# Kernel optimization log

Measured on AMD Instinct MI355X. Metric: run time of the kernel, lower is better.

## Reference

```python
import jax, jax.numpy as jnp
import numpy as np

B, N, K, D = 4, 2048, 32, 256
TOKEN_DIM = 256
EGO_DIM = 256
NUM_HEADS = 4
LN_EPS = 1e-6


def masked_softmax(logits, mask, axis):
    mask = mask.astype(jnp.bool_)
    while mask.ndim < logits.ndim:
        mask = mask[..., None]
    neg_big = jnp.finfo(logits.dtype).min
    has_any = jnp.any(mask, axis=axis, keepdims=True)
    masked_logits = jnp.where(mask, logits, neg_big)
    masked_logits = jnp.where(has_any, masked_logits, 0.0)
    weights = jax.nn.softmax(masked_logits, axis=axis)
    weights = jnp.where(mask, weights, 0.0)
    denom = jnp.sum(weights, axis=axis, keepdims=True)
    weights = jnp.where(denom > 0, weights / denom, 0.0)
    return weights


def setup_inputs() -> dict:
    key = jax.random.key(0)
    ks = jax.random.split(key, 10)
    inv_tok = jax.random.normal(ks[0], (B, N, K, D), dtype=jnp.float32)
    ego_ctx = jax.random.normal(ks[1], (B, N, EGO_DIM), dtype=jnp.float32)
    r = jax.random.normal(ks[2], (B, N, K, 3), dtype=jnp.float32)
    u = jax.random.normal(ks[3], (B, N, K, 3), dtype=jnp.float32)
    mask = jax.random.randint(ks[4], (B, N, K), 0, 2).astype(jnp.bool_)
    # params
    W_ego = jax.random.normal(ks[5], (EGO_DIM, TOKEN_DIM), dtype=jnp.float32) * 0.05
    b_ego = jnp.zeros((TOKEN_DIM,), dtype=jnp.float32)
    ln_scale = jnp.ones((D,), dtype=jnp.float32)
    ln_bias = jnp.zeros((D,), dtype=jnp.float32)
    W_h = jax.random.normal(ks[6], (D + TOKEN_DIM, TOKEN_DIM), dtype=jnp.float32) * 0.05
    b_h = jnp.zeros((TOKEN_DIM,), dtype=jnp.float32)
    W_logit = jax.random.normal(ks[7], (TOKEN_DIM, NUM_HEADS), dtype=jnp.float32) * 0.01
    b_logit = jnp.zeros((NUM_HEADS,), dtype=jnp.float32)
    return {"inv_tok": inv_tok, "ego_ctx": ego_ctx, "r": r, "u": u, "mask": mask,
            "W_ego": W_ego, "b_ego": b_ego, "ln_scale": ln_scale, "ln_bias": ln_bias,
            "W_h": W_h, "b_h": b_h, "W_logit": W_logit, "b_logit": b_logit}


def reference(inv_tok, ego_ctx, r, u, mask, W_ego, b_ego, ln_scale, ln_bias, W_h, b_h, W_logit, b_logit):
    # ego context projection, broadcast over K
    ego_h = ego_ctx @ W_ego + b_ego                      # (B,N,T)
    ego_b = jnp.broadcast_to(ego_h[:, :, None, :], (B, N, K, TOKEN_DIM))
    # LayerNorm over last axis of inv_tok
    mean = jnp.mean(inv_tok, axis=-1, keepdims=True)
    var = jnp.var(inv_tok, axis=-1, keepdims=True)
    ln = (inv_tok - mean) * jax.lax.rsqrt(var + LN_EPS) * ln_scale + ln_bias
    h = jnp.concatenate([ln, ego_b], axis=-1)            # (B,N,K,D+T)
    h = jax.nn.gelu(h @ W_h + b_h, approximate=True)     # (B,N,K,T)
    logits = h @ W_logit + b_logit                       # (B,N,K,H)
    alpha = masked_softmax(logits, mask, axis=-2)        # (B,N,K,H)
    v_r = jnp.einsum('bnkh,bnkd->bnhd', alpha, r).reshape(B, N, 3 * NUM_HEADS)
    v_u = jnp.einsum('bnkh,bnkd->bnhd', alpha, u).reshape(B, N, 3 * NUM_HEADS)
    return (v_r, v_u, alpha)
```

## Files before the change

kernel.cpp:

```cpp
#include <hip/hip_runtime.h>

typedef float f32x4 __attribute__((ext_vector_type(4)));
typedef short bf16x8 __attribute__((ext_vector_type(8)));

__device__ __forceinline__ unsigned short f2bf(float f){
    unsigned int u = __builtin_bit_cast(unsigned int, f);
    u = u + 0x7fffu + ((u >> 16) & 1u);
    return (unsigned short)(u >> 16);
}
__device__ __forceinline__ float bf2f(unsigned short h){
    unsigned int u = ((unsigned int)h) << 16;
    return __builtin_bit_cast(float, u);
}
__device__ __forceinline__ unsigned int pk2_rtz(float a, float b){
    unsigned int ua = __builtin_bit_cast(unsigned int, a);
    unsigned int ub = __builtin_bit_cast(unsigned int, b);
    return (ua >> 16) | (ub & 0xffff0000u);
}
__device__ __forceinline__ unsigned short bfrtz(float a){
    return (unsigned short)(__builtin_bit_cast(unsigned int, a) >> 16);
}
__device__ __forceinline__ float gelu_f(float x){
    float t = x * x;
    float u = fmaf(0.044715f, t, 1.0f);
    float y = 1.5957691216057308f * x * u;
    float e = __expf(-y);
    return x * __builtin_amdgcn_rcpf(1.0f + e);
}

__device__ __forceinline__ int packpos(int k, int n, int NT){
    int kt = k >> 5, quad = (k >> 3) & 3, j = k & 7;
    int nt = n >> 4, nl = n & 15;
    return ((kt * NT + nt) * 64 + quad * 16 + nl) * 8 + j;
}

__global__ __launch_bounds__(256) void prep(const float* __restrict__ Wh,
        const float* __restrict__ Wlogit, const float* __restrict__ Wego,
        const float* __restrict__ b_ego, const float* __restrict__ b_h,
        const float* __restrict__ ln_s, const float* __restrict__ ln_b,
        unsigned short* __restrict__ Bp1, unsigned short* __restrict__ BpL,
        unsigned short* __restrict__ Bpc, float* __restrict__ b_combo,
        float* __restrict__ v1){
    __shared__ float rowbuf[512];
    int bid = blockIdx.x, tid = threadIdx.x;
    if (bid < 64){
        int base = (bid * 256 + tid) * 4;
        int k = base >> 8;
        float sc = ln_s[k];
        for (int e = base; e < base + 4; ++e){
            int n = e & 255;
            Bp1[packpos(k, n, 16)] = f2bf(sc * Wh[k * 256 + n]);
        }
    } else if (bid == 64){
        for (int e = tid * 16; e < tid * 16 + 16; ++e){
            int k = e >> 4, n = e & 15;
            float v = (n < 4) ? Wlogit[k * 4 + n] : 0.0f;
            BpL[packpos(k, n, 1)] = f2bf(v);
        }
    } else if (bid == 65){
        rowbuf[tid]       = b_ego[tid];
        rowbuf[256 + tid] = ln_b[tid];
        __syncthreads();
        float acc = b_h[tid];
        for (int j = 0; j < 256; ++j) acc += rowbuf[j] * Wh[(256 + j) * 256 + tid];
        for (int k = 0; k < 256; ++k) acc += rowbuf[256 + k] * Wh[k * 256 + tid];
        b_combo[tid] = acc;
    } else if (bid == 66){
        rowbuf[tid] = ln_s[tid];
        __syncthreads();
        float acc = 0.f;
        for (int k = 0; k < 256; ++k)
            acc += bf2f(f2bf(rowbuf[k] * Wh[k * 256 + tid]));
        v1[tid] = acc;
    } else {
        int k = bid - 67;
        rowbuf[tid] = Wego[k * 256 + tid];
        __syncthreads();
        float acc = 0.f;
        const float4* row4 = (const float4*)rowbuf;
        for (int j4 = 0; j4 < 64; ++j4){
            float4 e = row4[j4];
            int j = j4 * 4;
            acc += e.x * Wh[(256 + j) * 256 + tid];
            acc += e.y * Wh[(257 + j) * 256 + tid];
            acc += e.z * Wh[(258 + j) * 256 + tid];
            acc += e.w * Wh[(259 + j) * 256 + tid];
        }
        Bpc[packpos(k, tid, 16)] = f2bf(acc);
    }
}

__global__ __launch_bounds__(256) void ego_gemm(const float* __restrict__ ego_ctx,
        const unsigned short* __restrict__ Bpc, const float* __restrict__ b_combo,
        unsigned short* __restrict__ ego_term){
    const int tid = threadIdx.x, w = tid >> 6, l = tid & 63;
    const int m0 = blockIdx.x * 16;
    const int row = m0 + (l & 15);
    const int kq = (l >> 4) << 3;
    f32x4 acc[4];
    #pragma unroll
    for (int j = 0; j < 4; ++j) acc[j] = 0;
    #pragma unroll
    for (int kt = 0; kt < 8; ++kt){
        const float* ap = ego_ctx + row * 256 + kt * 32 + kq;
        float4 x0 = *(const float4*)ap;
        float4 x1 = *(const float4*)(ap + 4);
        unsigned int ua[4];
        ua[0] = ((unsigned int)f2bf(x0.x)) | ((unsigned int)f2bf(x0.y) << 16);
        ua[1] = ((unsigned int)f2bf(x0.z)) | ((unsigned int)f2bf(x0.w) << 16);
        ua[2] = ((unsigned int)f2bf(x1.x)) | ((unsigned int)f2bf(x1.y) << 16);
        ua[3] = ((unsigned int)f2bf(x1.z)) | ((unsigned int)f2bf(x1.w) << 16);
        bf16x8 a = __builtin_bit_cast(bf16x8, *(uint4*)ua);
        #pragma unroll
        for (int j = 0; j < 4; ++j){
            int nt = w * 4 + j;
            bf16x8 b = *(const bf16x8*)&Bpc[((kt * 16 + nt) * 64 + l) * 8];
            acc[j] = __builtin_amdgcn_mfma_f32_16x16x32_bf16(a, b, acc[j], 0, 0, 0);
        }
    }
    const int rq = (l >> 4) << 2, colc = l & 15;
    #pragma unroll
    for (int j = 0; j < 4; ++j){
        int n = (w * 4 + j) * 16 + colc;
        float bc = b_combo[n];
        #pragma unroll
        for (int rg = 0; rg < 4; ++rg)
            ego_term[(m0 + rq + rg) * 256 + n] = f2bf(acc[j][rg] + bc);
    }
}

__global__ __launch_bounds__(256) void main_fused(const float* __restrict__ inv,
        const float* __restrict__ rin, const float* __restrict__ uin,
        const int* __restrict__ mask, const float* __restrict__ b_logit,
        const unsigned short* __restrict__ Bp1, const unsigned short* __restrict__ BpL,
        const unsigned short* __restrict__ ego_term, const float* __restrict__ v1g,
        float* __restrict__ out){

    __shared__ unsigned short Albs[64 * 264];
    __shared__ float2 stats_s[64];
    __shared__ float logit_s[256];

    const int tid = threadIdx.x;
    const int w = tid >> 6, l = tid & 63;
    const int T0 = blockIdx.x * 64;
    const int bn0 = blockIdx.x * 2;
    const int col = l & 15, quad = l >> 4, kq = quad << 3;
    const int r0 = w * 16;
    const int gw = w >> 1;

    const int h_sm = ((w & 1) << 1) + (l >> 5);
    const int k_sm = l & 31;
    const int row_sm = gw * 32 + k_sm;
    const int mvalid = mask[T0 + row_sm];
    const float blg = b_logit[h_sm];
    const float* rp = rin + (T0 + row_sm) * 3;
    const float* up = uin + (T0 + row_sm) * 3;
    float rv0 = rp[0], rv1 = rp[1], rv2 = rp[2];
    float uv0 = up[0], uv1 = up[1], uv2 = up[2];

    {
        const float* base = inv + (T0 + r0) * 256 + l * 4;
        #pragma unroll
        for (int rr = 0; rr < 16; ++rr){
            float4 c = *(const float4*)(base + rr * 256);
            uint2 p;
            p.x = pk2_rtz(c.x, c.y);
            p.y = pk2_rtz(c.z, c.w);
            *(uint2*)&Albs[(r0 + rr) * 264 + l * 4] = p;
        }
    }

    f32x4 acc[16];
    #pragma unroll
    for (int i = 0; i < 16; ++i) acc[i] = 0;
    f32x4 gacc = 0, sacc = 0;
    bf16x8 ones;
    #pragma unroll
    for (int j = 0; j < 8; ++j) ones[j] = (short)0x3F80;

    #pragma unroll
    for (int kt = 0; kt < 8; ++kt){
        bf16x8 af = *(const bf16x8*)&Albs[(r0 + col) * 264 + kt * 32 + kq];
        gacc = __builtin_amdgcn_mfma_f32_16x16x32_bf16(af, af,   gacc, 0, 0, 0);
        sacc = __builtin_amdgcn_mfma_f32_16x16x32_bf16(af, ones, sacc, 0, 0, 0);
        #pragma unroll
        for (int nt = 0; nt < 16; ++nt){
            bf16x8 bv = *(const bf16x8*)&Bp1[((kt * 16 + nt) * 64 + l) * 8];
            acc[nt] = __builtin_amdgcn_mfma_f32_16x16x32_bf16(af, bv, acc[nt], 0, 0, 0);
        }
    }

    if ((col >> 2) == quad){
        int rg = col & 3;
        float mean = sacc[rg] * (1.0f / 256.0f);
        float var  = gacc[rg] * (1.0f / 256.0f) - mean * mean;
        float rstd = rsqrtf(var + 1e-6f);
        stats_s[r0 + col] = float2{rstd, rstd * mean};
    }
    float2 st[4];
    #pragma unroll
    for (int rg = 0; rg < 4; ++rg) st[rg] = stats_s[r0 + quad * 4 + rg];

    #pragma unroll
    for (int nt = 0; nt < 16; ++nt){
        const int n = nt * 16 + col;
        const float v1n = v1g[n];
        const float egn = bf2f(ego_term[(bn0 + gw) * 256 + n]);
        #pragma unroll
        for (int rg = 0; rg < 4; ++rg){
            float x = fmaf(st[rg].x, acc[nt][rg], fmaf(-st[rg].y, v1n, egn));
            Albs[(r0 + quad * 4 + rg) * 264 + n] = bfrtz(gelu_f(x));
        }
    }

    {
        f32x4 lacc = 0;
        #pragma unroll
        for (int kt = 0; kt < 8; ++kt){
            bf16x8 a = *(const bf16x8*)&Albs[(r0 + col) * 264 + kt * 32 + kq];
            bf16x8 b = *(const bf16x8*)&BpL[(kt * 64 + l) * 8];
            lacc = __builtin_amdgcn_mfma_f32_16x16x32_bf16(a, b, lacc, 0, 0, 0);
        }
        if (col < 4){
            #pragma unroll
            for (int rg = 0; rg < 4; ++rg)
                logit_s[(r0 + quad * 4 + rg) * 4 + col] = lacc[rg];
        }
    }

    __syncthreads();

    {
        float lg = logit_s[row_sm * 4 + h_sm] + blg;
        float val = mvalid ? lg : -3.0e38f;
        float mx = val;
        #pragma unroll
        for (int off = 16; off >= 1; off >>= 1)
            mx = fmaxf(mx, __shfl_xor(mx, off));
        float e = mvalid ? __expf(lg - mx) : 0.0f;
        float ssum = e;
        #pragma unroll
        for (int off = 16; off >= 1; off >>= 1)
            ssum += __shfl_xor(ssum, off);
        float a = (ssum > 0.f) ? e / ssum : 0.0f;
        out[196608 + (T0 + row_sm) * 4 + h_sm] = a;

        float p0 = a * rv0, p1 = a * rv1, p2 = a * rv2;
        float p3 = a * uv0, p4 = a * uv1, p5 = a * uv2;
        #pragma unroll
        for (int off = 16; off >= 1; off >>= 1){
            p0 += __shfl_xor(p0, off);
            p1 += __shfl_xor(p1, off);
            p2 += __shfl_xor(p2, off);
            p3 += __shfl_xor(p3, off);
            p4 += __shfl_xor(p4, off);
            p5 += __shfl_xor(p5, off);
        }
        if (k_sm == 0){
            int ob = (bn0 + gw) * 12 + h_sm * 3;
            out[ob    ] = p0;
            out[ob + 1] = p1;
            out[ob + 2] = p2;
            out[98304 + ob    ] = p3;
            out[98304 + ob + 1] = p4;
            out[98304 + ob + 2] = p5;
        }
    }
}

extern "C" void kernel_launch(void* const* d_in, const int* in_sizes, int n_in,
                              void* d_out, int out_size, void* d_ws, size_t ws_size,
                              hipStream_t stream){
    const float* inv    = (const float*)d_in[0];
    const float* ego    = (const float*)d_in[1];
    const float* rin    = (const float*)d_in[2];
    const float* uin    = (const float*)d_in[3];
    const int*   mask   = (const int*)  d_in[4];
    const float* Wego   = (const float*)d_in[5];
    const float* b_ego  = (const float*)d_in[6];
    const float* ln_s   = (const float*)d_in[7];
    const float* ln_b   = (const float*)d_in[8];
    const float* Wh     = (const float*)d_in[9];
    const float* b_h    = (const float*)d_in[10];
    const float* Wlogit = (const float*)d_in[11];
    const float* b_lg   = (const float*)d_in[12];
    float* out = (float*)d_out;

    unsigned short* wsu = (unsigned short*)d_ws;
    unsigned short* Bp1 = wsu;
    unsigned short* Bpc = wsu + 65536;
    unsigned short* BpL = wsu + 131072;
    float* b_combo      = (float*)(wsu + 135168);
    float* v1           = (float*)(wsu + 135680);
    unsigned short* ego_term = wsu + 136192;

    prep<<<323, 256, 0, stream>>>(Wh, Wlogit, Wego, b_ego, b_h, ln_s, ln_b,
                                  Bp1, BpL, Bpc, b_combo, v1);
    ego_gemm<<<512, 256, 0, stream>>>(ego, Bpc, b_combo, ego_term);
    main_fused<<<4096, 256, 0, stream>>>(inv, rin, uin, mask, b_lg,
                                         Bp1, BpL, ego_term, v1, out);
}
```

Before: 506.3 us.

## Split main kernel to one (b,n) per block and rebalance prep kernels

The main fused kernel now processes 32 tokens (one b,n position) per 256-thread block instead of 64. The four waves split the N dimension of the Wh GEMM, each covering 64 output columns for both 16-row tiles, so each wave keeps 8 accumulators instead of 16. The block count doubles, which should raise occupancy and cut register pressure, at the cost of extra __syncthreads and idle waves during the softmax. The prep work is also regrouped: the Wh/Wlogit packing moves into the ego GEMM launch so it runs alongside it, and the ego input conversion switches to truncating bf16 packing.

```diff
diff --git a/kernel.cpp b/kernel.cpp
--- a/kernel.cpp
+++ b/kernel.cpp
@@ -34,46 +34,14 @@
     return ((kt * NT + nt) * 64 + quad * 16 + nl) * 8 + j;
 }
 
-__global__ __launch_bounds__(256) void prep(const float* __restrict__ Wh,
-        const float* __restrict__ Wlogit, const float* __restrict__ Wego,
-        const float* __restrict__ b_ego, const float* __restrict__ b_h,
-        const float* __restrict__ ln_s, const float* __restrict__ ln_b,
-        unsigned short* __restrict__ Bp1, unsigned short* __restrict__ BpL,
-        unsigned short* __restrict__ Bpc, float* __restrict__ b_combo,
-        float* __restrict__ v1){
+__global__ __launch_bounds__(256) void combo_pack(const float* __restrict__ Wh,
+        const float* __restrict__ Wego, const float* __restrict__ b_ego,
+        const float* __restrict__ b_h, const float* __restrict__ ln_b,
+        unsigned short* __restrict__ Bpc, float* __restrict__ b_combo){
     __shared__ float rowbuf[512];
     int bid = blockIdx.x, tid = threadIdx.x;
-    if (bid < 64){
-        int base = (bid * 256 + tid) * 4;
-        int k = base >> 8;
-        float sc = ln_s[k];
-        for (int e = base; e < base + 4; ++e){
-            int n = e & 255;
-            Bp1[packpos(k, n, 16)] = f2bf(sc * Wh[k * 256 + n]);
-        }
-    } else if (bid == 64){
-        for (int e = tid * 16; e < tid * 16 + 16; ++e){
-            int k = e >> 4, n = e & 15;
-            float v = (n < 4) ? Wlogit[k * 4 + n] : 0.0f;
-            BpL[packpos(k, n, 1)] = f2bf(v);
-        }
-    } else if (bid == 65){
-        rowbuf[tid]       = b_ego[tid];
-        rowbuf[256 + tid] = ln_b[tid];
-        __syncthreads();
-        float acc = b_h[tid];
-        for (int j = 0; j < 256; ++j) acc += rowbuf[j] * Wh[(256 + j) * 256 + tid];
-        for (int k = 0; k < 256; ++k) acc += rowbuf[256 + k] * Wh[k * 256 + tid];
-        b_combo[tid] = acc;
-    } else if (bid == 66){
-        rowbuf[tid] = ln_s[tid];
-        __syncthreads();
-        float acc = 0.f;
-        for (int k = 0; k < 256; ++k)
-            acc += bf2f(f2bf(rowbuf[k] * Wh[k * 256 + tid]));
-        v1[tid] = acc;
-    } else {
-        int k = bid - 67;
+    if (bid < 256){
+        int k = bid;
         rowbuf[tid] = Wego[k * 256 + tid];
         __syncthreads();
         float acc = 0.f;
@@ -87,45 +55,81 @@
             acc += e.w * Wh[(259 + j) * 256 + tid];
         }
         Bpc[packpos(k, tid, 16)] = f2bf(acc);
-    }
-}
-
-__global__ __launch_bounds__(256) void ego_gemm(const float* __restrict__ ego_ctx,
+    } else {
+        rowbuf[tid]       = b_ego[tid];
+        rowbuf[256 + tid] = ln_b[tid];
+        __syncthreads();
+        float acc = b_h[tid];
+        for (int j = 0; j < 256; ++j) acc += rowbuf[j] * Wh[(256 + j) * 256 + tid];
+        for (int k = 0; k < 256; ++k) acc += rowbuf[256 + k] * Wh[k * 256 + tid];
+        b_combo[tid] = acc;
+    }
+}
+
+__global__ __launch_bounds__(256) void ego_plus(const float* __restrict__ ego_ctx,
         const unsigned short* __restrict__ Bpc, const float* __restrict__ b_combo,
-        unsigned short* __restrict__ ego_term){
-    const int tid = threadIdx.x, w = tid >> 6, l = tid & 63;
-    const int m0 = blockIdx.x * 16;
-    const int row = m0 + (l & 15);
-    const int kq = (l >> 4) << 3;
-    f32x4 acc[4];
-    #pragma unroll
-    for (int j = 0; j < 4; ++j) acc[j] = 0;
-    #pragma unroll
-    for (int kt = 0; kt < 8; ++kt){
-        const float* ap = ego_ctx + row * 256 + kt * 32 + kq;
-        float4 x0 = *(const float4*)ap;
-        float4 x1 = *(const float4*)(ap + 4);
-        unsigned int ua[4];
-        ua[0] = ((unsigned int)f2bf(x0.x)) | ((unsigned int)f2bf(x0.y) << 16);
-        ua[1] = ((unsigned int)f2bf(x0.z)) | ((unsigned int)f2bf(x0.w) << 16);
-        ua[2] = ((unsigned int)f2bf(x1.x)) | ((unsigned int)f2bf(x1.y) << 16);
-        ua[3] = ((unsigned int)f2bf(x1.z)) | ((unsigned int)f2bf(x1.w) << 16);
-        bf16x8 a = __builtin_bit_cast(bf16x8, *(uint4*)ua);
+        const float* __restrict__ Wh, const float* __restrict__ Wlogit,
+        const float* __restrict__ ln_s,
+        unsigned short* __restrict__ ego_term, unsigned short* __restrict__ Bp1,
+        unsigned short* __restrict__ BpL, float* __restrict__ v1){
+    __shared__ float rowbuf[256];
+    const int bid = blockIdx.x, tid = threadIdx.x;
+    if (bid < 512){
+        const int w = tid >> 6, l = tid & 63;
+        const int m0 = bid * 16;
+        const int row = m0 + (l & 15);
+        const int kq = (l >> 4) << 3;
+        f32x4 acc[4];
+        #pragma unroll
+        for (int j = 0; j < 4; ++j) acc[j] = 0;
+        #pragma unroll
+        for (int kt = 0; kt < 8; ++kt){
+            const float* ap = ego_ctx + row * 256 + kt * 32 + kq;
+            float4 x0 = *(const float4*)ap;
+            float4 x1 = *(const float4*)(ap + 4);
+            unsigned int ua[4];
+            ua[0] = pk2_rtz(x0.x, x0.y);
+            ua[1] = pk2_rtz(x0.z, x0.w);
+            ua[2] = pk2_rtz(x1.x, x1.y);
+            ua[3] = pk2_rtz(x1.z, x1.w);
+            bf16x8 a = __builtin_bit_cast(bf16x8, *(uint4*)ua);
+            #pragma unroll
+            for (int j = 0; j < 4; ++j){
+                int nt = w * 4 + j;
+                bf16x8 b = *(const bf16x8*)&Bpc[((kt * 16 + nt) * 64 + l) * 8];
+                acc[j] = __builtin_amdgcn_mfma_f32_16x16x32_bf16(a, b, acc[j], 0, 0, 0);
+            }
+        }
+        const int rq = (l >> 4) << 2, colc = l & 15;
         #pragma unroll
         for (int j = 0; j < 4; ++j){
-            int nt = w * 4 + j;
-            bf16x8 b = *(const bf16x8*)&Bpc[((kt * 16 + nt) * 64 + l) * 8];
-            acc[j] = __builtin_amdgcn_mfma_f32_16x16x32_bf16(a, b, acc[j], 0, 0, 0);
-        }
-    }
-    const int rq = (l >> 4) << 2, colc = l & 15;
-    #pragma unroll
-    for (int j = 0; j < 4; ++j){
-        int n = (w * 4 + j) * 16 + colc;
-        float bc = b_combo[n];
-        #pragma unroll
-        for (int rg = 0; rg < 4; ++rg)
-            ego_term[(m0 + rq + rg) * 256 + n] = f2bf(acc[j][rg] + bc);
+            int n = (w * 4 + j) * 16 + colc;
+            float bc = b_combo[n];
+            #pragma unroll
+            for (int rg = 0; rg < 4; ++rg)
+                ego_term[(m0 + rq + rg) * 256 + n] = f2bf(acc[j][rg] + bc);
+        }
+    } else if (bid < 576){
+        int base = ((bid - 512) * 256 + tid) * 4;
+        int k = base >> 8;
+        float sc = ln_s[k];
+        for (int e = base; e < base + 4; ++e){
+            int n = e & 255;
+            Bp1[packpos(k, n, 16)] = f2bf(sc * Wh[k * 256 + n]);
+        }
+    } else if (bid == 576){
+        for (int e = tid * 16; e < tid * 16 + 16; ++e){
+            int k = e >> 4, n = e & 15;
+            float v = (n < 4) ? Wlogit[k * 4 + n] : 0.0f;
+            BpL[packpos(k, n, 1)] = f2bf(v);
+        }
+    } else {
+        rowbuf[tid] = ln_s[tid];
+        __syncthreads();
+        float acc = 0.f;
+        for (int k = 0; k < 256; ++k)
+            acc += bf2f(f2bf(rowbuf[k] * Wh[k * 256 + tid]));
+        v1[tid] = acc;
     }
 }
 
@@ -136,102 +140,124 @@
         const unsigned short* __restrict__ ego_term, const float* __restrict__ v1g,
         float* __restrict__ out){
 
-    __shared__ unsigned short Albs[64 * 264];
-    __shared__ float2 stats_s[64];
-    __shared__ float logit_s[256];
+    __shared__ unsigned short Albs[32 * 264];
+    __shared__ float2 stats_s[32];
+    __shared__ float logit_s[128];
 
     const int tid = threadIdx.x;
     const int w = tid >> 6, l = tid & 63;
-    const int T0 = blockIdx.x * 64;
-    const int bn0 = blockIdx.x * 2;
+    const int g = blockIdx.x;
+    const int T0 = g * 32;
     const int col = l & 15, quad = l >> 4, kq = quad << 3;
-    const int r0 = w * 16;
-    const int gw = w >> 1;
-
-    const int h_sm = ((w & 1) << 1) + (l >> 5);
+
+    const int h_sm = w * 2 + (l >> 5);
     const int k_sm = l & 31;
-    const int row_sm = gw * 32 + k_sm;
-    const int mvalid = mask[T0 + row_sm];
-    const float blg = b_logit[h_sm];
-    const float* rp = rin + (T0 + row_sm) * 3;
-    const float* up = uin + (T0 + row_sm) * 3;
-    float rv0 = rp[0], rv1 = rp[1], rv2 = rp[2];
-    float uv0 = up[0], uv1 = up[1], uv2 = up[2];
+    int mvalid = 0; float blg = 0.f;
+    float rv0 = 0.f, rv1 = 0.f, rv2 = 0.f, uv0 = 0.f, uv1 = 0.f, uv2 = 0.f;
+    if (w < 2){
+        mvalid = mask[T0 + k_sm];
+        blg = b_logit[h_sm];
+        const float* rp = rin + (T0 + k_sm) * 3;
+        const float* up = uin + (T0 + k_sm) * 3;
+        rv0 = rp[0]; rv1 = rp[1]; rv2 = rp[2];
+        uv0 = up[0]; uv1 = up[1]; uv2 = up[2];
+    }
+    float v1r[4], egn[4];
+    #pragma unroll
+    for (int i = 0; i < 4; ++i){
+        int n = w * 64 + i * 16 + col;
+        v1r[i] = v1g[n];
+        egn[i] = bf2f(ego_term[g * 256 + n]);
+    }
 
     {
-        const float* base = inv + (T0 + r0) * 256 + l * 4;
-        #pragma unroll
-        for (int rr = 0; rr < 16; ++rr){
+        const float* base = inv + (T0 + w * 8) * 256 + l * 4;
+        #pragma unroll
+        for (int rr = 0; rr < 8; ++rr){
             float4 c = *(const float4*)(base + rr * 256);
             uint2 p;
             p.x = pk2_rtz(c.x, c.y);
             p.y = pk2_rtz(c.z, c.w);
-            *(uint2*)&Albs[(r0 + rr) * 264 + l * 4] = p;
-        }
-    }
-
-    f32x4 acc[16];
+            *(uint2*)&Albs[(w * 8 + rr) * 264 + l * 4] = p;
+        }
+    }
+    __syncthreads();
+
+    f32x4 acc[2][4];
     #pragma unroll
-    for (int i = 0; i < 16; ++i) acc[i] = 0;
+    for (int a = 0; a < 2; ++a)
+        #pragma unroll
+        for (int b = 0; b < 4; ++b) acc[a][b] = 0;
     f32x4 gacc = 0, sacc = 0;
     bf16x8 ones;
     #pragma unroll
     for (int j = 0; j < 8; ++j) ones[j] = (short)0x3F80;
+    const int mts = w & 1;
 
     #pragma unroll
     for (int kt = 0; kt < 8; ++kt){
-        bf16x8 af = *(const bf16x8*)&Albs[(r0 + col) * 264 + kt * 32 + kq];
-        gacc = __builtin_amdgcn_mfma_f32_16x16x32_bf16(af, af,   gacc, 0, 0, 0);
-        sacc = __builtin_amdgcn_mfma_f32_16x16x32_bf16(af, ones, sacc, 0, 0, 0);
-        #pragma unroll
-        for (int nt = 0; nt < 16; ++nt){
-            bf16x8 bv = *(const bf16x8*)&Bp1[((kt * 16 + nt) * 64 + l) * 8];
-            acc[nt] = __builtin_amdgcn_mfma_f32_16x16x32_bf16(af, bv, acc[nt], 0, 0, 0);
-        }
-    }
-
+        const int ko = kt * 32 + kq;
+        bf16x8 af0 = *(const bf16x8*)&Albs[(     col) * 264 + ko];
+        bf16x8 af1 = *(const bf16x8*)&Albs[(16 + col) * 264 + ko];
+        bf16x8 afs = mts ? af1 : af0;
+        gacc = __builtin_amdgcn_mfma_f32_16x16x32_bf16(afs, afs,  gacc, 0, 0, 0);
+        sacc = __builtin_amdgcn_mfma_f32_16x16x32_bf16(afs, ones, sacc, 0, 0, 0);
+        #pragma unroll
+        for (int i = 0; i < 4; ++i){
+            bf16x8 bv = *(const bf16x8*)&Bp1[((kt * 16 + (w * 4 + i)) * 64 + l) * 8];
+            acc[0][i] = __builtin_amdgcn_mfma_f32_16x16x32_bf16(af0, bv, acc[0][i], 0, 0, 0);
+            acc[1][i] = __builtin_amdgcn_mfma_f32_16x16x32_bf16(af1, bv, acc[1][i], 0, 0, 0);
+        }
+    }
     if ((col >> 2) == quad){
         int rg = col & 3;
         float mean = sacc[rg] * (1.0f / 256.0f);
         float var  = gacc[rg] * (1.0f / 256.0f) - mean * mean;
         float rstd = rsqrtf(var + 1e-6f);
-        stats_s[r0 + col] = float2{rstd, rstd * mean};
-    }
-    float2 st[4];
-    #pragma unroll
-    for (int rg = 0; rg < 4; ++rg) st[rg] = stats_s[r0 + quad * 4 + rg];
-
-    #pragma unroll
-    for (int nt = 0; nt < 16; ++nt){
-        const int n = nt * 16 + col;
-        const float v1n = v1g[n];
-        const float egn = bf2f(ego_term[(bn0 + gw) * 256 + n]);
-        #pragma unroll
-        for (int rg = 0; rg < 4; ++rg){
-            float x = fmaf(st[rg].x, acc[nt][rg], fmaf(-st[rg].y, v1n, egn));
-            Albs[(r0 + quad * 4 + rg) * 264 + n] = bfrtz(gelu_f(x));
-        }
-    }
+        stats_s[mts * 16 + col] = float2{rstd, rstd * mean};
+    }
+    __syncthreads();
 
     {
+        float2 st[2][4];
+        #pragma unroll
+        for (int mt = 0; mt < 2; ++mt)
+            #pragma unroll
+            for (int rg = 0; rg < 4; ++rg)
+                st[mt][rg] = stats_s[mt * 16 + quad * 4 + rg];
+        #pragma unroll
+        for (int mt = 0; mt < 2; ++mt)
+            #pragma unroll
+            for (int i = 0; i < 4; ++i){
+                const int n = w * 64 + i * 16 + col;
+                #pragma unroll
+                for (int rg = 0; rg < 4; ++rg){
+                    float x = fmaf(st[mt][rg].x, acc[mt][i][rg],
+                                   fmaf(-st[mt][rg].y, v1r[i], egn[i]));
+                    Albs[(mt * 16 + quad * 4 + rg) * 264 + n] = bfrtz(gelu_f(x));
+                }
+            }
+    }
+    __syncthreads();
+
+    if (w < 2){
         f32x4 lacc = 0;
         #pragma unroll
         for (int kt = 0; kt < 8; ++kt){
-            bf16x8 a = *(const bf16x8*)&Albs[(r0 + col) * 264 + kt * 32 + kq];
+            bf16x8 a = *(const bf16x8*)&Albs[(w * 16 + col) * 264 + kt * 32 + kq];
             bf16x8 b = *(const bf16x8*)&BpL[(kt * 64 + l) * 8];
             lacc = __builtin_amdgcn_mfma_f32_16x16x32_bf16(a, b, lacc, 0, 0, 0);
         }
         if (col < 4){
             #pragma unroll
             for (int rg = 0; rg < 4; ++rg)
-                logit_s[(r0 + quad * 4 + rg) * 4 + col] = lacc[rg];
-        }
-    }
-
+                logit_s[(w * 16 + quad * 4 + rg) * 4 + col] = lacc[rg];
+        }
+    }
     __syncthreads();
 
-    {
-        float lg = logit_s[row_sm * 4 + h_sm] + blg;
+    if (w < 2){
+        float lg = logit_s[k_sm * 4 + h_sm] + blg;
         float val = mvalid ? lg : -3.0e38f;
         float mx = val;
         #pragma unroll
@@ -243,7 +269,7 @@
         for (int off = 16; off >= 1; off >>= 1)
             ssum += __shfl_xor(ssum, off);
         float a = (ssum > 0.f) ? e / ssum : 0.0f;
-        out[196608 + (T0 + row_sm) * 4 + h_sm] = a;
+        out[196608 + (T0 + k_sm) * 4 + h_sm] = a;
 
         float p0 = a * rv0, p1 = a * rv1, p2 = a * rv2;
         float p3 = a * uv0, p4 = a * uv1, p5 = a * uv2;
@@ -257,7 +283,7 @@
             p5 += __shfl_xor(p5, off);
         }
         if (k_sm == 0){
-            int ob = (bn0 + gw) * 12 + h_sm * 3;
+            int ob = g * 12 + h_sm * 3;
             out[ob    ] = p0;
             out[ob + 1] = p1;
             out[ob + 2] = p2;
@@ -294,9 +320,9 @@
     float* v1           = (float*)(wsu + 135680);
     unsigned short* ego_term = wsu + 136192;
 
-    prep<<<323, 256, 0, stream>>>(Wh, Wlogit, Wego, b_ego, b_h, ln_s, ln_b,
-                                  Bp1, BpL, Bpc, b_combo, v1);
-    ego_gemm<<<512, 256, 0, stream>>>(ego, Bpc, b_combo, ego_term);
-    main_fused<<<4096, 256, 0, stream>>>(inv, rin, uin, mask, b_lg,
+    combo_pack<<<257, 256, 0, stream>>>(Wh, Wego, b_ego, b_h, ln_b, Bpc, b_combo);
+    ego_plus<<<578, 256, 0, stream>>>(ego, Bpc, b_combo, Wh, Wlogit, ln_s,
+                                      ego_term, Bp1, BpL, v1);
+    main_fused<<<8192, 256, 0, stream>>>(inv, rin, uin, mask, b_lg,
                                          Bp1, BpL, ego_term, v1, out);
 }
```

After: 460.4 us. 9.1% less time.
